# Kernel optimization log

Hardware: AMD Instinct MI355X
Metric: run time of the kernel (lower is better)

## Reference

```python
import jax, jax.numpy as jnp
import numpy as np

B, L, D, H = 2, 2048, 1024, 16
HD = D // H  # 64


def rotate_half(x):
    x1, x2 = x[..., : x.shape[-1] // 2], x[..., x.shape[-1] // 2 :]
    return jnp.concatenate([-x2, x1], axis=-1)


def apply_rope(x, cos, sin):
    # x: (B, H, L, HD); cos/sin: (1, L, HD)
    c = cos[:, None, : x.shape[2], :]
    s = sin[:, None, : x.shape[2], :]
    return x * c + rotate_half(x) * s


def setup_inputs() -> dict:
    key = jax.random.key(0)
    ks = jax.random.split(key, 16)
    query = jax.random.normal(ks[0], (B, L, D), jnp.float32)
    k_in = jax.random.normal(ks[1], (B, L, D), jnp.float32)
    v_in = jax.random.normal(ks[2], (B, L, D), jnp.float32)
    key_padding_mask = jax.random.uniform(ks[3], (B, L)) < 0.2
    # genuine RoPE tables
    inv_freq = 1.0 / (10000.0 ** (jnp.arange(0, HD, 2, dtype=jnp.float32) / HD))
    ang = jnp.arange(L, dtype=jnp.float32)[:, None] * inv_freq[None, :]  # (L, HD/2)
    ang = jnp.concatenate([ang, ang], axis=-1)  # (L, HD)
    rope_cos = jnp.cos(ang)[None]  # (1, L, HD)
    rope_sin = jnp.sin(ang)[None]
    scale = 0.02
    Wq = jax.random.normal(ks[4], (D, D), jnp.float32) * scale
    bq = jnp.zeros((D,), jnp.float32)
    Wk = jax.random.normal(ks[5], (D, D), jnp.float32) * scale
    bk = jnp.zeros((D,), jnp.float32)
    Wv = jax.random.normal(ks[6], (D, D), jnp.float32) * scale
    bv = jnp.zeros((D,), jnp.float32)
    Wg = jax.random.normal(ks[7], (D, D), jnp.float32) * scale  # init zeros in torch; random for grad coverage
    bg = jnp.ones((D,), jnp.float32)
    Wo = jax.random.normal(ks[8], (D, D), jnp.float32) * scale
    bo = jnp.zeros((D,), jnp.float32)
    return dict(query=query, key=k_in, value=v_in, key_padding_mask=key_padding_mask,
                rope_cos=rope_cos, rope_sin=rope_sin,
                Wq=Wq, bq=bq, Wk=Wk, bk=bk, Wv=Wv, bv=bv,
                Wg=Wg, bg=bg, Wo=Wo, bo=bo)


def reference(query, key, value, key_padding_mask, rope_cos, rope_sin,
              Wq, bq, Wk, bk, Wv, bv, Wg, bg, Wo, bo):
    Bq, Lq, _ = query.shape
    Lk = key.shape[1]
    # torch Linear: x @ W.T + b
    Q = (query @ Wq.T + bq).reshape(Bq, Lq, H, HD).transpose(0, 2, 1, 3)
    K = (key @ Wk.T + bk).reshape(Bq, Lk, H, HD).transpose(0, 2, 1, 3)
    V = (value @ Wv.T + bv).reshape(Bq, Lk, H, HD).transpose(0, 2, 1, 3)
    K = apply_rope(K, rope_cos, rope_sin)
    Q = apply_rope(Q, rope_cos, rope_sin)
    scale = 1.0 / jnp.sqrt(jnp.asarray(HD, query.dtype))
    scores = jnp.einsum('bhqd,bhkd->bhqk', Q, K) * scale
    allow = ~key_padding_mask[:, None, None, :]  # (B,1,1,Lk): True = attend
    scores = jnp.where(allow, scores, -jnp.inf)
    attn = jax.nn.softmax(scores, axis=-1)
    out = jnp.einsum('bhqk,bhkd->bhqd', attn, V)
    out = jnp.nan_to_num(out, nan=0.0)
    out = out.transpose(0, 2, 1, 3).reshape(Bq, Lq, D)
    gate = jax.nn.sigmoid(query @ Wg.T + bg)
    out = out * gate
    out = out @ Wo.T + bo
    return out
```

## Files before the change

### kernel.cpp

```cpp
#include <hip/hip_runtime.h>
#include <hip/hip_bf16.h>
#include <cstdint>


constexpr int NB = 2, NL = 2048, ND = 1024, NH = 16, NHD = 64;
constexpr int NM = NB * NL;

typedef __bf16 bf16_t;
typedef __bf16 bf16x8 __attribute__((ext_vector_type(8)));
typedef __bf16 bf16x4 __attribute__((ext_vector_type(4)));
typedef float f32x4 __attribute__((ext_vector_type(4)));
typedef float f32x16 __attribute__((ext_vector_type(16)));
typedef unsigned int uint2v __attribute__((ext_vector_type(2)));

typedef const __attribute__((address_space(1))) void* gas_ptr;
typedef __attribute__((address_space(3))) void* las_ptr;

__device__ __forceinline__ void async_load16(const void* g, void* l) {
  __builtin_amdgcn_global_load_lds((gas_ptr)g, (las_ptr)l, 16, 0, 0);
}

__device__ __forceinline__ unsigned cvtpk_bf16(float lo, float hi) {
  unsigned r;
  asm("v_cvt_pk_bf16_f32 %0, %1, %2" : "=v"(r) : "v"(lo), "v"(hi));
  return r;
}

__device__ __forceinline__ void pl32_swap(unsigned& a, unsigned& b) {
#if __has_builtin(__builtin_amdgcn_permlane32_swap)
  uint2v r = __builtin_amdgcn_permlane32_swap(a, b, false, false);
  a = r.x; b = r.y;
#else
  asm volatile("v_permlane32_swap_b32 %0, %1" : "+v"(a), "+v"(b));
#endif
}

__device__ __forceinline__ float fast_exp2(float x) {
#if __has_builtin(__builtin_amdgcn_exp2f)
  return __builtin_amdgcn_exp2f(x);
#else
  float r;
  asm("v_exp_f32 %0, %1" : "=v"(r) : "v"(x));
  return r;
#endif
}

struct CvtArgs {
  const float* s[8];
  bf16_t* d[8];
  const float* rc;
  const float* rs;
  bf16_t* pt;
};
__global__ __launch_bounds__(256) void cvt8_kernel(CvtArgs a) {
  int y = blockIdx.y;
  if (y == 8) {
    int n = NL * 16;
    for (int i = blockIdx.x * 256 + threadIdx.x; i < n; i += gridDim.x * 256) {
      int l = i >> 4, lr = i & 15;
      const float* c = a.rc + l * NHD + lr;
      const float* s = a.rs + l * NHD + lr;
      bf16x8 o;
      o[0] = (bf16_t)c[0];  o[1] = (bf16_t)c[16];
      o[2] = (bf16_t)c[32]; o[3] = (bf16_t)c[48];
      o[4] = (bf16_t)s[0];  o[5] = (bf16_t)s[16];
      o[6] = (bf16_t)s[32]; o[7] = (bf16_t)s[48];
      ((bf16x8*)a.pt)[i] = o;
    }
    return;
  }
  int n4 = (y < 3) ? (NM * ND / 4) : (ND * ND / 4);
  const float* src = a.s[y];
  bf16_t* dst = a.d[y];
  for (int i = blockIdx.x * 256 + threadIdx.x; i < n4; i += gridDim.x * 256) {
    float4 v = ((const float4*)src)[i];
    bf16x4 o;
    o[0] = (bf16_t)v.x; o[1] = (bf16_t)v.y; o[2] = (bf16_t)v.z; o[3] = (bf16_t)v.w;
    ((bf16x4*)dst)[i] = o;
  }
}

__global__ __launch_bounds__(512, 2) void gemm8_kernel(
    const bf16_t* __restrict__ Aq, const bf16_t* __restrict__ Ak, const bf16_t* __restrict__ Av,
    const bf16_t* __restrict__ W0, const bf16_t* __restrict__ W1,
    const bf16_t* __restrict__ W2, const bf16_t* __restrict__ W3,
    const float* __restrict__ b0, const float* __restrict__ b1,
    const float* __restrict__ b2, const float* __restrict__ b3,
    const bf16_t* __restrict__ PT,
    bf16_t* __restrict__ Qr, bf16_t* __restrict__ Kr, bf16_t* __restrict__ Vt,
    bf16_t* __restrict__ Gb) {
  extern __shared__ __align__(16) bf16_t smem[];
  bf16_t* lA = smem;
  bf16_t* lB = smem + 32768;

  const int tid = threadIdx.x, lane = tid & 63, w = tid >> 6;
  const int wm = w >> 2, wn = w & 3;
  const int lr = lane & 15, lg = lane >> 4;

  const int lin = blockIdx.x;
  const int xcd = lin & 7, idx = lin >> 3;
  const int nt = xcd * 2 + (idx & 1);
  const int mt = idx >> 1;
  const int t = nt >> 2;
  const bf16_t* Asrc = (t == 1) ? Ak : (t == 2) ? Av : Aq;
  const bf16_t* Wsrc = (t == 0) ? W0 : (t == 1) ? W1 : (t == 2) ? W2 : W3;
  const int nbase = (nt & 3) * 256;

  const int srow = lane >> 3;
  const int gcol = ((lane & 7) ^ srow) * 8;

  auto stageA = [&](int buf, int hf, int kt) {
#pragma unroll
    for (int jj = 0; jj < 2; ++jj) {
      int slot = jj * 8 + w;
      int r = slot * 8 + srow;
      async_load16(Asrc + (size_t)(mt * 256 + hf * 128 + r) * ND + kt * 64 + gcol,
                   lA + (buf * 2 + hf) * 8192 + slot * 512);
    }
  };
  auto stageB = [&](int buf, int hf, int kt) {
#pragma unroll
    for (int jj = 0; jj < 2; ++jj) {
      int slot = jj * 8 + w;
      int r = slot * 8 + srow;
      async_load16(Wsrc + (size_t)(nbase + hf * 128 + r) * ND + kt * 64 + gcol,
                   lB + (buf * 2 + hf) * 8192 + slot * 512);
    }
  };

  f32x4 acc[8][4];
#pragma unroll
  for (int i = 0; i < 8; ++i)
#pragma unroll
    for (int j = 0; j < 4; ++j)
#pragma unroll
      for (int k = 0; k < 4; ++k) acc[i][j][k] = 0.f;

  stageA(0, 0, 0); stageA(0, 1, 0); stageB(0, 0, 0); stageB(0, 1, 0);
  stageB(1, 0, 1); stageB(1, 1, 1);
  asm volatile("s_waitcnt vmcnt(4)" ::: "memory");
  __builtin_amdgcn_s_barrier();

  const bf16_t* Ab[2] = { lA + wm * 8192, lA + (2 + wm) * 8192 };
  const bf16_t* Bb[2] = { lB + (wn >> 1) * 8192 + (wn & 1) * 4096,
                          lB + (2 + (wn >> 1)) * 8192 + (wn & 1) * 4096 };

  for (int j = 0; j < 8; ++j) {
#pragma unroll
    for (int hp = 0; hp < 2; ++hp) {
      const bf16_t* Ap = Ab[hp];
      const bf16_t* Bp = Bb[hp];
      bf16x8 bfr[4][2];
#pragma unroll
      for (int p = 0; p < 4; ++p) {
        bf16x8 af[2][2];
#pragma unroll
        for (int mi = 0; mi < 2; ++mi)
#pragma unroll
          for (int ks = 0; ks < 2; ++ks)
            af[mi][ks] = *(const bf16x8*)(Ap + ((p * 2 + mi) * 16 + lr) * 64 +
                                          ((ks * 4 + lg) ^ (lr & 7)) * 8);
        if (p == 0) {
#pragma unroll
          for (int nj = 0; nj < 4; ++nj)
#pragma unroll
            for (int ks = 0; ks < 2; ++ks)
              bfr[nj][ks] = *(const bf16x8*)(Bp + (nj * 16 + lr) * 64 +
                                             ((ks * 4 + lg) ^ (lr & 7)) * 8);
        }
        if (hp == 0) {
          if (p == 0) stageA(1, 0, 2 * j + 1);
          if (p == 1) { stageA(1, 1, 2 * j + 1); if (j < 7) stageB(0, 0, 2 * j + 2); }
          if (p == 2) { if (j < 7) stageB(0, 1, 2 * j + 2); }
        } else if (j < 7) {
          if (p == 0) stageA(0, 0, 2 * j + 2);
          if (p == 1) { stageA(0, 1, 2 * j + 2); stageB(1, 0, 2 * j + 3); }
          if (p == 2) stageB(1, 1, 2 * j + 3);
        }
        __builtin_amdgcn_s_barrier();
        __builtin_amdgcn_s_setprio(1);
#pragma unroll
        for (int mi = 0; mi < 2; ++mi)
#pragma unroll
          for (int nj = 0; nj < 4; ++nj)
#pragma unroll
            for (int ks = 0; ks < 2; ++ks)
              acc[p * 2 + mi][nj] = __builtin_amdgcn_mfma_f32_16x16x32_bf16(
                  af[mi][ks], bfr[nj][ks], acc[p * 2 + mi][nj], 0, 0, 0);
        __builtin_amdgcn_s_setprio(0);
        if (p == 3) {
          if (hp == 0) {
            if (j < 7) { asm volatile("s_waitcnt vmcnt(4)" ::: "memory"); }
            else       { asm volatile("s_waitcnt vmcnt(0)" ::: "memory"); }
          } else if (j < 7) {
            asm volatile("s_waitcnt vmcnt(4)" ::: "memory");
          }
        }
        __builtin_amdgcn_s_barrier();
      }
    }
  }

  const int fbase = nbase + wn * 64;
  const int h = fbase >> 6;
  if (t < 2) {
    bf16_t* dst = (t == 0) ? Qr : Kr;
    const float* bias = (t == 0) ? b0 : b1;
    const float qs = (t == 0) ? 0.18033688011112042f : 1.0f;
    float bl[4];
#pragma unroll
    for (int d4 = 0; d4 < 4; ++d4) bl[d4] = bias[fbase + d4 * 16 + lr];
#pragma unroll
    for (int i = 0; i < 8; ++i)
#pragma unroll
      for (int rg = 0; rg < 4; ++rg) {
        int mm = mt * 256 + wm * 128 + i * 16 + lg * 4 + rg;
        int bb = mm >> 11, l = mm & (NL - 1);
        bf16_t* rowp = dst + ((bb * NH + h) * NL + l) * NHD;
        bf16x8 pk8 = *(const bf16x8*)(PT + (l * 16 + lr) * 8);
#pragma unroll
        for (int nj = 0; nj < 2; ++nj) {
          int dlo = nj * 16 + lr, dhi = dlo + 32;
          float clo = (float)pk8[nj],     chi = (float)pk8[nj + 2];
          float slo = (float)pk8[nj + 4], shi = (float)pk8[nj + 6];
          float xlo = acc[i][nj][rg] + bl[nj];
          float xhi = acc[i][nj + 2][rg] + bl[nj + 2];
          rowp[dlo] = (bf16_t)((xlo * clo - xhi * slo) * qs);
          rowp[dhi] = (bf16_t)((xhi * chi + xlo * shi) * qs);
        }
      }
  } else if (t == 2) {
    float bl[4];
#pragma unroll
    for (int d4 = 0; d4 < 4; ++d4) bl[d4] = b2[fbase + d4 * 16 + lr];
#pragma unroll
    for (int i = 0; i < 8; ++i) {
      int mmb = mt * 256 + wm * 128 + i * 16 + lg * 4;
      int bb = mmb >> 11, l0 = mmb & (NL - 1);
#pragma unroll
      for (int nj = 0; nj < 4; ++nj) {
        int d = nj * 16 + lr;
        float bias = bl[nj];
        unsigned u01 = cvtpk_bf16(acc[i][nj][0] + bias, acc[i][nj][1] + bias);
        unsigned u23 = cvtpk_bf16(acc[i][nj][2] + bias, acc[i][nj][3] + bias);
        unsigned long long pk = (unsigned long long)u01 | ((unsigned long long)u23 << 32);
        *(unsigned long long*)(Vt + ((bb * NH + h) * NHD + d) * NL + l0) = pk;
      }
    }
  } else {
    float bl[4];
#pragma unroll
    for (int d4 = 0; d4 < 4; ++d4) bl[d4] = b3[fbase + d4 * 16 + lr];
#pragma unroll
    for (int i = 0; i < 8; ++i)
#pragma unroll
      for (int rg = 0; rg < 4; ++rg) {
        int mm = mt * 256 + wm * 128 + i * 16 + lg * 4 + rg;
#pragma unroll
        for (int nj = 0; nj < 4; ++nj) {
          int f = fbase + nj * 16 + lr;
          Gb[mm * ND + f] = (bf16_t)(acc[i][nj][rg] + bl[nj]);
        }
      }
  }
}

__global__ __launch_bounds__(256) void gemm_out_kernel(
    const bf16_t* __restrict__ A, const bf16_t* __restrict__ W,
    const float* __restrict__ bias0, float* __restrict__ Out) {
  __shared__ __align__(16) bf16_t lA[2][128 * 64];
  __shared__ __align__(16) bf16_t lB[2][128 * 64];
  const int tid = threadIdx.x, lane = tid & 63, w = tid >> 6;
  const int wm = w >> 1, wn = w & 1;
  const int lr = lane & 15, lg = lane >> 4;

  const int lin = blockIdx.x;
  const int ntile = lin & 7, mtile = lin >> 3;

  const bf16_t* Ablk = A + mtile * 128 * ND;
  const bf16_t* Wblk = W + ntile * 128 * ND;

  f32x4 acc[4][4];
#pragma unroll
  for (int i = 0; i < 4; ++i)
#pragma unroll
    for (int j = 0; j < 4; ++j)
#pragma unroll
      for (int k = 0; k < 4; ++k) acc[i][j][k] = 0.f;

  auto STAGE = [&](int b, int kb) {
#pragma unroll
    for (int p = 0; p < 4; ++p) {
      int q = w * 256 + p * 64 + lane;
      int r = q >> 3, c = q & 7;
      int cs = c ^ (r & 7);
      async_load16(Ablk + r * ND + kb * 64 + cs * 8, &lA[b][(w * 256 + p * 64) * 8]);
      async_load16(Wblk + r * ND + kb * 64 + cs * 8, &lB[b][(w * 256 + p * 64) * 8]);
    }
  };
  auto COMPUTE = [&](int b) {
    const bf16_t* pA = lA[b];
    const bf16_t* pB = lB[b];
#pragma unroll
    for (int ks = 0; ks < 2; ++ks) {
      bf16x8 af[4], bfr[4];
#pragma unroll
      for (int i = 0; i < 4; ++i) {
        int ra = wm * 64 + i * 16 + lr;
        int ca = (ks * 4 + lg) ^ (ra & 7);
        af[i] = *(const bf16x8*)(pA + ra * 64 + ca * 8);
        int rb = wn * 64 + i * 16 + lr;
        int cb = (ks * 4 + lg) ^ (rb & 7);
        bfr[i] = *(const bf16x8*)(pB + rb * 64 + cb * 8);
      }
#pragma unroll
      for (int i = 0; i < 4; ++i)
#pragma unroll
        for (int j = 0; j < 4; ++j)
          acc[i][j] = __builtin_amdgcn_mfma_f32_16x16x32_bf16(af[i], bfr[j], acc[i][j], 0, 0, 0);
    }
  };

  STAGE(0, 0);
  __syncthreads();
  int buf = 0;
  for (int kb = 0; kb < 15; ++kb) {
    STAGE(buf ^ 1, kb + 1);
    COMPUTE(buf);
    __syncthreads();
    buf ^= 1;
  }
  COMPUTE(buf);

#pragma unroll
  for (int j = 0; j < 4; ++j) {
    int nn = ntile * 128 + wn * 64 + j * 16 + lr;
    float bias = bias0[nn];
#pragma unroll
    for (int i = 0; i < 4; ++i)
#pragma unroll
      for (int rg = 0; rg < 4; ++rg) {
        int mm = mtile * 128 + wm * 64 + i * 16 + lg * 4 + rg;
        Out[mm * ND + nn] = acc[i][j][rg] + bias;
      }
  }
}

__global__ __launch_bounds__(256) void attn_kernel(
    const bf16_t* __restrict__ Qr, const bf16_t* __restrict__ Kr, const bf16_t* __restrict__ Vt,
    const int* __restrict__ mask, const bf16_t* __restrict__ Gb, bf16_t* __restrict__ X) {
  __shared__ __align__(16) bf16_t lK[2][128 * 64];
  __shared__ __align__(16) bf16_t lV[2][64 * 128];

  int lin = blockIdx.y * gridDim.x + blockIdx.x;
  int swz = (lin & 7) * 64 + (lin >> 3);
  const int qb = swz & 15, bh = swz >> 4;
  const int bb = bh >> 4, h = bh & 15;

  const int tid = threadIdx.x, lane = tid & 63, w = tid >> 6;
  const int ql = lane & 31, hi = lane >> 5;

  const bf16_t* Kbh = Kr + bh * NL * NHD;
  const bf16_t* Vbh = Vt + bh * NHD * NL;
  const int q = qb * 128 + w * 32 + ql;

  const bf16_t* Qp = Qr + (bh * NL + q) * NHD + 8 * hi;
  bf16x8 qf[4];
#pragma unroll
  for (int c = 0; c < 4; ++c) qf[c] = *(const bf16x8*)(Qp + 16 * c);
  bf16x8 qf5 = {};
  qf5[0] = (bf16_t)(hi ? 0.f : 1.f);

  f32x16 zero16;
#pragma unroll
  for (int r = 0; r < 16; ++r) zero16[r] = 0.f;
  bf16x8 ones8;
#pragma unroll
  for (int r = 0; r < 8; ++r) ones8[r] = (bf16_t)1.f;

  f32x16 acc[2];
#pragma unroll
  for (int dt = 0; dt < 2; ++dt)
#pragma unroll
    for (int r = 0; r < 16; ++r) acc[dt][r] = 0.f;
  f32x16 lacc16 = zero16;

  const bf16_t* gsrc[8];
#pragma unroll
  for (int j = 0; j < 8; ++j) {
    if (j < 4) {
      int u = j * 256 + tid;
      int r = u >> 3, c = u & 7, cs = c ^ (r & 7);
      gsrc[j] = Kbh + r * NHD + cs * 8;
    } else {
      int v = (j - 4) * 256 + tid;
      int r = v >> 4, c = v & 15, cs = (c & 8) | ((c & 7) ^ (r & 7));
      gsrc[j] = Vbh + r * NL + cs * 8;
    }
  }
  auto STAGE = [&](int b) {
#pragma unroll
    for (int j = 0; j < 8; ++j) {
      if (j < 4) {
        async_load16(gsrc[j], &lK[b][(j * 256 + tid) * 8]);
        gsrc[j] += 128 * NHD;
      } else {
        async_load16(gsrc[j], &lV[b][((j - 4) * 256 + tid) * 8]);
        gsrc[j] += 128;
      }
    }
  };

  unsigned rdK[2][4], rdV[2][4];
#pragma unroll
  for (int t2 = 0; t2 < 2; ++t2)
#pragma unroll
    for (int c = 0; c < 4; ++c) {
      unsigned un = ((2 * c + hi) ^ (ql & 7)) * 16;
      rdK[t2][c] = (32 * t2 + ql) * 128 + un;
      rdV[t2][c] = (32 * t2 + ql) * 256 + un;
    }
  const char* lKc = (const char*)lK;
  const char* lVc = (const char*)lV;

  STAGE(0);
  int mv0 = mask[bb * NL + lane];
  int mv1 = mask[bb * NL + 64 + lane];
  __syncthreads();

  auto BODY = [&](int buf, int t) {
    int nmv0 = 0, nmv1 = 0;
    if (t < 15) {
      STAGE(buf ^ 1);
      nmv0 = mask[bb * NL + (t + 1) * 128 + lane];
      nmv1 = mask[bb * NL + (t + 1) * 128 + 64 + lane];
    }
    unsigned long long bmA = __ballot(mv0 != 0);
    unsigned long long bmB = __ballot(mv1 != 0);
    unsigned mws[4] = {(unsigned)bmA, (unsigned)(bmA >> 32),
                       (unsigned)bmB, (unsigned)(bmB >> 32)};
    bf16x8 kf5[4];
#pragma unroll
    for (int g = 0; g < 4; ++g) {
      float bv = ((mws[g] >> ql) & 1u) ? -1008.f : -8.f;
      bf16x8 z = {};
      z[0] = (bf16_t)(hi ? 0.f : bv);
      kf5[g] = z;
    }
#pragma unroll
    for (int hh = 0; hh < 2; ++hh) {
      f32x16 st[2];
      __builtin_amdgcn_s_setprio(1);
#pragma unroll
      for (int t2 = 0; t2 < 2; ++t2) {
        f32x16 s = __builtin_amdgcn_mfma_f32_32x32x16_bf16(kf5[hh * 2 + t2], qf5,
                                                           zero16, 0, 0, 0);
#pragma unroll
        for (int c = 0; c < 4; ++c) {
          bf16x8 kf = *(const bf16x8*)(lKc + rdK[t2][c] + buf * 16384 + hh * 8192);
          s = __builtin_amdgcn_mfma_f32_32x32x16_bf16(kf, qf[c], s, 0, 0, 0);
        }
        st[t2] = s;
      }
      __builtin_amdgcn_s_setprio(0);

#pragma unroll
      for (int t2 = 0; t2 < 2; ++t2)
#pragma unroll
        for (int r = 0; r < 16; ++r) st[t2][r] = fast_exp2(st[t2][r]);

      unsigned wds[2][4][2];
#pragma unroll
      for (int t2 = 0; t2 < 2; ++t2)
#pragma unroll
        for (int r1 = 0; r1 < 4; ++r1) {
          wds[t2][r1][0] = cvtpk_bf16(st[t2][4 * r1 + 0], st[t2][4 * r1 + 1]);
          wds[t2][r1][1] = cvtpk_bf16(st[t2][4 * r1 + 2], st[t2][4 * r1 + 3]);
        }
      bf16x8 pf[4];
#pragma unroll
      for (int kc = 0; kc < 4; ++kc) {
        int t2 = kc >> 1, r1a = 2 * (kc & 1);
        unsigned a0 = wds[t2][r1a][0], b0 = wds[t2][r1a + 1][0];
        unsigned a1 = wds[t2][r1a][1], b1 = wds[t2][r1a + 1][1];
        pl32_swap(a0, b0);
        pl32_swap(a1, b1);
        union { unsigned u[4]; bf16x8 v; } uu;
        uu.u[0] = a0; uu.u[1] = a1; uu.u[2] = b0; uu.u[3] = b1;
        pf[kc] = uu.v;
      }

      __builtin_amdgcn_s_setprio(1);
#pragma unroll
      for (int dt = 0; dt < 2; ++dt) {
        f32x16 a = acc[dt];
#pragma unroll
        for (int kc = 0; kc < 4; ++kc) {
          bf16x8 vf = *(const bf16x8*)(lVc + rdV[dt][kc] + buf * 16384 + hh * 128);
          a = __builtin_amdgcn_mfma_f32_32x32x16_bf16(vf, pf[kc], a, 0, 0, 0);
        }
        acc[dt] = a;
      }
#pragma unroll
      for (int kc = 0; kc < 4; ++kc)
        lacc16 = __builtin_amdgcn_mfma_f32_32x32x16_bf16(ones8, pf[kc], lacc16, 0, 0, 0);
      __builtin_amdgcn_s_setprio(0);
    }
    __syncthreads();
    mv0 = nmv0;
    mv1 = nmv1;
  };

  for (int tt = 0; tt < 8; ++tt) {
    BODY(0, 2 * tt);
    BODY(1, 2 * tt + 1);
  }

  float lt = lacc16[0];
  float rinv = lt > 0.f ? 1.f / lt : 0.f;
  const int rowbase = (bb * NL + q) * ND + h * NHD;
#pragma unroll
  for (int dt = 0; dt < 2; ++dt)
#pragma unroll
    for (int r1 = 0; r1 < 4; ++r1) {
      int dbase = 32 * dt + 8 * r1 + 4 * hi;
      bf16x4 g4 = *(const bf16x4*)(Gb + rowbase + dbase);
      bf16x4 o;
#pragma unroll
      for (int j = 0; j < 4; ++j) {
        float gate = 1.f / (1.f + fast_exp2(-1.44269504f * (float)g4[j]));
        o[j] = (bf16_t)(acc[dt][4 * r1 + j] * rinv * gate);
      }
      *(bf16x4*)(X + rowbase + dbase) = o;
    }
}

extern "C" void kernel_launch(void* const* d_in, const int* in_sizes, int n_in,
                              void* d_out, int out_size, void* d_ws, size_t ws_size,
                              hipStream_t stream) {
  const float* query = (const float*)d_in[0];
  const float* key   = (const float*)d_in[1];
  const float* value = (const float*)d_in[2];
  const int*   maskp = (const int*)d_in[3];
  const float* rcos  = (const float*)d_in[4];
  const float* rsin  = (const float*)d_in[5];
  const float* Wq = (const float*)d_in[6];  const float* bq = (const float*)d_in[7];
  const float* Wk = (const float*)d_in[8];  const float* bk = (const float*)d_in[9];
  const float* Wv = (const float*)d_in[10]; const float* bv = (const float*)d_in[11];
  const float* Wg = (const float*)d_in[12]; const float* bg = (const float*)d_in[13];
  const float* Wo = (const float*)d_in[14]; const float* bo = (const float*)d_in[15];

  constexpr size_t MB = 1ull << 20;
  char* ws = (char*)d_ws;
  bf16_t* qbb = (bf16_t*)(ws + 0 * MB);
  bf16_t* kbb = (bf16_t*)(ws + 8 * MB);
  bf16_t* vbb = (bf16_t*)(ws + 16 * MB);
  bf16_t* wqb = (bf16_t*)(ws + 24 * MB);
  bf16_t* wkb = (bf16_t*)(ws + 26 * MB);
  bf16_t* wvb = (bf16_t*)(ws + 28 * MB);
  bf16_t* wgb = (bf16_t*)(ws + 30 * MB);
  bf16_t* wob = (bf16_t*)(ws + 32 * MB);
  bf16_t* Qr  = (bf16_t*)(ws + 34 * MB);
  bf16_t* Kr  = (bf16_t*)(ws + 42 * MB);
  bf16_t* Vt  = (bf16_t*)(ws + 50 * MB);
  bf16_t* Gb  = (bf16_t*)(ws + 58 * MB);
  bf16_t* PT  = (bf16_t*)(ws + 66 * MB);
  bf16_t* Xb  = (bf16_t*)(ws + 74 * MB);

  CvtArgs ca;
  ca.s[0] = query; ca.d[0] = qbb;
  ca.s[1] = key;   ca.d[1] = kbb;
  ca.s[2] = value; ca.d[2] = vbb;
  ca.s[3] = Wq;    ca.d[3] = wqb;
  ca.s[4] = Wk;    ca.d[4] = wkb;
  ca.s[5] = Wv;    ca.d[5] = wvb;
  ca.s[6] = Wg;    ca.d[6] = wgb;
  ca.s[7] = Wo;    ca.d[7] = wob;
  ca.rc = rcos; ca.rs = rsin; ca.pt = PT;
  cvt8_kernel<<<dim3(1024, 9), 256, 0, stream>>>(ca);

  gemm8_kernel<<<256, 512, 131072, stream>>>(
      qbb, kbb, vbb, wqb, wkb, wvb, wgb, bq, bk, bv, bg, PT,
      Qr, Kr, Vt, Gb);

  attn_kernel<<<dim3(16, 32), 256, 0, stream>>>(Qr, Kr, Vt, maskp, Gb, Xb);

  gemm_out_kernel<<<256, 256, 0, stream>>>(Xb, wob, bo, (float*)d_out);
}
```

Measured before the change: 131.7 us.

## Load K/V fragments straight from global into registers, dropping LDS staging

The attention kernel no longer stages K and V tiles through double-buffered shared memory with async global-to-LDS loads and block barriers. Each wave now loads its MFMA operand fragments directly from global memory into registers, prefetching the next K tile one iteration ahead, and steps through 64-key tiles. The row-sum is built with VALU adds plus a cross-half shuffle instead of an extra ones-MFMA, and the mask bias changes from -1008/-8 to -1000/0. This removes LDS traffic and __syncthreads, but each of the four waves now fetches the same K/V data separately from global/L2 and raises register pressure.

New measurement: 197.6 us. 50.0% more time.

```diff
diff --git a/kernel.cpp b/kernel.cpp
--- a/kernel.cpp
+++ b/kernel.cpp
@@ -349,9 +349,6 @@
 __global__ __launch_bounds__(256) void attn_kernel(
     const bf16_t* __restrict__ Qr, const bf16_t* __restrict__ Kr, const bf16_t* __restrict__ Vt,
     const int* __restrict__ mask, const bf16_t* __restrict__ Gb, bf16_t* __restrict__ X) {
-  __shared__ __align__(16) bf16_t lK[2][128 * 64];
-  __shared__ __align__(16) bf16_t lV[2][64 * 128];
-
   int lin = blockIdx.y * gridDim.x + blockIdx.x;
   int swz = (lin & 7) * 64 + (lin >> 3);
   const int qb = swz & 15, bh = swz >> 4;
@@ -359,9 +356,6 @@
 
   const int tid = threadIdx.x, lane = tid & 63, w = tid >> 6;
   const int ql = lane & 31, hi = lane >> 5;
-
-  const bf16_t* Kbh = Kr + bh * NL * NHD;
-  const bf16_t* Vbh = Vt + bh * NHD * NL;
   const int q = qb * 128 + w * 32 + ql;
 
   const bf16_t* Qp = Qr + (bh * NL + q) * NHD + 8 * hi;
@@ -374,150 +368,116 @@
   f32x16 zero16;
 #pragma unroll
   for (int r = 0; r < 16; ++r) zero16[r] = 0.f;
-  bf16x8 ones8;
-#pragma unroll
-  for (int r = 0; r < 8; ++r) ones8[r] = (bf16_t)1.f;
 
   f32x16 acc[2];
 #pragma unroll
   for (int dt = 0; dt < 2; ++dt)
 #pragma unroll
     for (int r = 0; r < 16; ++r) acc[dt][r] = 0.f;
-  f32x16 lacc16 = zero16;
-
-  const bf16_t* gsrc[8];
-#pragma unroll
-  for (int j = 0; j < 8; ++j) {
-    if (j < 4) {
-      int u = j * 256 + tid;
-      int r = u >> 3, c = u & 7, cs = c ^ (r & 7);
-      gsrc[j] = Kbh + r * NHD + cs * 8;
-    } else {
-      int v = (j - 4) * 256 + tid;
-      int r = v >> 4, c = v & 15, cs = (c & 8) | ((c & 7) ^ (r & 7));
-      gsrc[j] = Vbh + r * NL + cs * 8;
-    }
-  }
-  auto STAGE = [&](int b) {
-#pragma unroll
-    for (int j = 0; j < 8; ++j) {
-      if (j < 4) {
-        async_load16(gsrc[j], &lK[b][(j * 256 + tid) * 8]);
-        gsrc[j] += 128 * NHD;
-      } else {
-        async_load16(gsrc[j], &lV[b][((j - 4) * 256 + tid) * 8]);
-        gsrc[j] += 128;
-      }
-    }
+  f32x4 lacc = {0.f, 0.f, 0.f, 0.f};
+
+  const bf16_t* kbase = Kr + (size_t)bh * NL * NHD + ql * NHD + hi * 8;
+  const bf16_t* vbase = Vt + (size_t)bh * NHD * NL + ql * NL + hi * 8;
+  const int* mp = mask + bb * NL + lane;
+
+  bf16x8 kc_[8], kn_[8], vv_[8];
+
+  auto LOADK = [&](bf16x8* dst, int t) {
+#pragma unroll
+    for (int t2 = 0; t2 < 2; ++t2)
+#pragma unroll
+      for (int c = 0; c < 4; ++c)
+        dst[t2 * 4 + c] = *(const bf16x8*)(kbase + t * 64 * NHD + t2 * 32 * NHD + c * 16);
   };
-
-  unsigned rdK[2][4], rdV[2][4];
-#pragma unroll
-  for (int t2 = 0; t2 < 2; ++t2)
-#pragma unroll
-    for (int c = 0; c < 4; ++c) {
-      unsigned un = ((2 * c + hi) ^ (ql & 7)) * 16;
-      rdK[t2][c] = (32 * t2 + ql) * 128 + un;
-      rdV[t2][c] = (32 * t2 + ql) * 256 + un;
-    }
-  const char* lKc = (const char*)lK;
-  const char* lVc = (const char*)lV;
-
-  STAGE(0);
-  int mv0 = mask[bb * NL + lane];
-  int mv1 = mask[bb * NL + 64 + lane];
-  __syncthreads();
-
-  auto BODY = [&](int buf, int t) {
-    int nmv0 = 0, nmv1 = 0;
-    if (t < 15) {
-      STAGE(buf ^ 1);
-      nmv0 = mask[bb * NL + (t + 1) * 128 + lane];
-      nmv1 = mask[bb * NL + (t + 1) * 128 + 64 + lane];
-    }
-    unsigned long long bmA = __ballot(mv0 != 0);
-    unsigned long long bmB = __ballot(mv1 != 0);
-    unsigned mws[4] = {(unsigned)bmA, (unsigned)(bmA >> 32),
-                       (unsigned)bmB, (unsigned)(bmB >> 32)};
-    bf16x8 kf5[4];
-#pragma unroll
-    for (int g = 0; g < 4; ++g) {
-      float bv = ((mws[g] >> ql) & 1u) ? -1008.f : -8.f;
-      bf16x8 z = {};
-      z[0] = (bf16_t)(hi ? 0.f : bv);
-      kf5[g] = z;
-    }
-#pragma unroll
-    for (int hh = 0; hh < 2; ++hh) {
-      f32x16 st[2];
-      __builtin_amdgcn_s_setprio(1);
-#pragma unroll
-      for (int t2 = 0; t2 < 2; ++t2) {
-        f32x16 s = __builtin_amdgcn_mfma_f32_32x32x16_bf16(kf5[hh * 2 + t2], qf5,
-                                                           zero16, 0, 0, 0);
-#pragma unroll
-        for (int c = 0; c < 4; ++c) {
-          bf16x8 kf = *(const bf16x8*)(lKc + rdK[t2][c] + buf * 16384 + hh * 8192);
-          s = __builtin_amdgcn_mfma_f32_32x32x16_bf16(kf, qf[c], s, 0, 0, 0);
-        }
-        st[t2] = s;
-      }
-      __builtin_amdgcn_s_setprio(0);
-
-#pragma unroll
-      for (int t2 = 0; t2 < 2; ++t2)
-#pragma unroll
-        for (int r = 0; r < 16; ++r) st[t2][r] = fast_exp2(st[t2][r]);
-
-      unsigned wds[2][4][2];
-#pragma unroll
-      for (int t2 = 0; t2 < 2; ++t2)
-#pragma unroll
-        for (int r1 = 0; r1 < 4; ++r1) {
-          wds[t2][r1][0] = cvtpk_bf16(st[t2][4 * r1 + 0], st[t2][4 * r1 + 1]);
-          wds[t2][r1][1] = cvtpk_bf16(st[t2][4 * r1 + 2], st[t2][4 * r1 + 3]);
-        }
-      bf16x8 pf[4];
-#pragma unroll
-      for (int kc = 0; kc < 4; ++kc) {
-        int t2 = kc >> 1, r1a = 2 * (kc & 1);
-        unsigned a0 = wds[t2][r1a][0], b0 = wds[t2][r1a + 1][0];
-        unsigned a1 = wds[t2][r1a][1], b1 = wds[t2][r1a + 1][1];
-        pl32_swap(a0, b0);
-        pl32_swap(a1, b1);
-        union { unsigned u[4]; bf16x8 v; } uu;
-        uu.u[0] = a0; uu.u[1] = a1; uu.u[2] = b0; uu.u[3] = b1;
-        pf[kc] = uu.v;
-      }
-
-      __builtin_amdgcn_s_setprio(1);
-#pragma unroll
-      for (int dt = 0; dt < 2; ++dt) {
-        f32x16 a = acc[dt];
-#pragma unroll
-        for (int kc = 0; kc < 4; ++kc) {
-          bf16x8 vf = *(const bf16x8*)(lVc + rdV[dt][kc] + buf * 16384 + hh * 128);
-          a = __builtin_amdgcn_mfma_f32_32x32x16_bf16(vf, pf[kc], a, 0, 0, 0);
-        }
-        acc[dt] = a;
-      }
+  auto LOADV = [&](bf16x8* dst, int t) {
+#pragma unroll
+    for (int dt = 0; dt < 2; ++dt)
 #pragma unroll
       for (int kc = 0; kc < 4; ++kc)
-        lacc16 = __builtin_amdgcn_mfma_f32_32x32x16_bf16(ones8, pf[kc], lacc16, 0, 0, 0);
-      __builtin_amdgcn_s_setprio(0);
-    }
-    __syncthreads();
-    mv0 = nmv0;
-    mv1 = nmv1;
+        dst[dt * 4 + kc] = *(const bf16x8*)(vbase + dt * 32 * NL + t * 64 + kc * 16);
   };
 
-  for (int tt = 0; tt < 8; ++tt) {
-    BODY(0, 2 * tt);
-    BODY(1, 2 * tt + 1);
-  }
-
-  float lt = lacc16[0];
+  LOADK(kc_, 0);
+  int mvc = mp[0];
+
+  for (int t = 0; t < 32; ++t) {
+    LOADV(vv_, t);
+    int mvn = 0;
+    if (t < 31) {
+      LOADK(kn_, t + 1);
+      mvn = mp[(t + 1) * 64];
+    }
+    unsigned long long bm = __ballot(mvc != 0);
+    unsigned mw[2] = {(unsigned)bm, (unsigned)(bm >> 32)};
+
+    f32x16 st[2];
+    __builtin_amdgcn_s_setprio(1);
+#pragma unroll
+    for (int t2 = 0; t2 < 2; ++t2) {
+      bf16x8 k5 = {};
+      k5[0] = (bf16_t)(hi ? 0.f : (((mw[t2] >> ql) & 1u) ? -1000.f : 0.f));
+      f32x16 s = __builtin_amdgcn_mfma_f32_32x32x16_bf16(k5, qf5, zero16, 0, 0, 0);
+#pragma unroll
+      for (int c = 0; c < 4; ++c)
+        s = __builtin_amdgcn_mfma_f32_32x32x16_bf16(kc_[t2 * 4 + c], qf[c], s, 0, 0, 0);
+      st[t2] = s;
+    }
+    __builtin_amdgcn_s_setprio(0);
+
+#pragma unroll
+    for (int t2 = 0; t2 < 2; ++t2)
+#pragma unroll
+      for (int r = 0; r < 16; ++r) st[t2][r] = fast_exp2(st[t2][r]);
+#pragma unroll
+    for (int t2 = 0; t2 < 2; ++t2)
+#pragma unroll
+      for (int r4 = 0; r4 < 4; ++r4) {
+        f32x4 pv = {st[t2][4 * r4 + 0], st[t2][4 * r4 + 1],
+                    st[t2][4 * r4 + 2], st[t2][4 * r4 + 3]};
+        lacc += pv;
+      }
+
+    unsigned wds[2][4][2];
+#pragma unroll
+    for (int t2 = 0; t2 < 2; ++t2)
+#pragma unroll
+      for (int r1 = 0; r1 < 4; ++r1) {
+        wds[t2][r1][0] = cvtpk_bf16(st[t2][4 * r1 + 0], st[t2][4 * r1 + 1]);
+        wds[t2][r1][1] = cvtpk_bf16(st[t2][4 * r1 + 2], st[t2][4 * r1 + 3]);
+      }
+    bf16x8 pf[4];
+#pragma unroll
+    for (int kc = 0; kc < 4; ++kc) {
+      int t2 = kc >> 1, r1a = 2 * (kc & 1);
+      unsigned a0 = wds[t2][r1a][0], b0 = wds[t2][r1a + 1][0];
+      unsigned a1 = wds[t2][r1a][1], b1 = wds[t2][r1a + 1][1];
+      pl32_swap(a0, b0);
+      pl32_swap(a1, b1);
+      union { unsigned u[4]; bf16x8 v; } uu;
+      uu.u[0] = a0; uu.u[1] = a1; uu.u[2] = b0; uu.u[3] = b1;
+      pf[kc] = uu.v;
+    }
+
+    __builtin_amdgcn_s_setprio(1);
+#pragma unroll
+    for (int dt = 0; dt < 2; ++dt) {
+      f32x16 a = acc[dt];
+#pragma unroll
+      for (int kc = 0; kc < 4; ++kc)
+        a = __builtin_amdgcn_mfma_f32_32x32x16_bf16(vv_[dt * 4 + kc], pf[kc], a, 0, 0, 0);
+      acc[dt] = a;
+    }
+    __builtin_amdgcn_s_setprio(0);
+
+#pragma unroll
+    for (int i = 0; i < 8; ++i) kc_[i] = kn_[i];
+    mvc = mvn;
+  }
+
+  float lt = lacc[0] + lacc[1] + lacc[2] + lacc[3];
+  lt += __shfl_xor(lt, 32, 64);
   float rinv = lt > 0.f ? 1.f / lt : 0.f;
+
   const int rowbase = (bb * NL + q) * ND + h * NHD;
 #pragma unroll
   for (int dt = 0; dt < 2; ++dt)
```
